# Optimization experiments

Measured on AMD Instinct MI355X. Metric: run time of the kernel, lower is better.

The kernel has to match this reference:

```python
import jax, jax.numpy as jnp
import numpy as np

K = 2
BN_EPS = 1e-5


def setup_inputs() -> dict:
    key = jax.random.key(0)
    k1, k2, k3 = jax.random.split(key, 3)
    B, C, H, W, D, O = 4, 128, 32, 32, 32, 128
    x = jax.random.normal(k1, (B, C, H, W, D), dtype=jnp.float32)
    conv_w = jax.random.normal(k2, (O, 2 * C), dtype=jnp.float32) * 0.02  # 1x1x1 conv kernel
    conv_b = jax.random.normal(k3, (O,), dtype=jnp.float32) * 0.02
    bn_gamma = jnp.ones((O,), dtype=jnp.float32)
    bn_beta = jnp.zeros((O,), dtype=jnp.float32)
    return {"x": x, "conv_w": conv_w, "conv_b": conv_b,
            "bn_gamma": bn_gamma, "bn_beta": bn_beta}


def _axis_running_max(x, x_j, axis, dim):
    # torch.cat([x[..., -i:], x[..., :-i]], axis) == jnp.roll(x, i, axis)
    shifts = jnp.arange(K, dim, K)

    def step(carry, s):
        diff = x - jnp.roll(x, s, axis=axis)
        return jnp.maximum(carry, diff), None

    x_j, _ = jax.lax.scan(step, x_j, shifts)
    return x_j


def reference(x, conv_w, conv_b, bn_gamma, bn_beta):
    B, C, H, W, D = x.shape
    x_j = jnp.zeros_like(x)
    x_j = _axis_running_max(x, x_j, 2, H)
    x_j = _axis_running_max(x, x_j, 3, W)
    x_j = _axis_running_max(x, x_j, 4, D)
    x_j = jax.lax.stop_gradient(x_j)  # original detaches every x_j update

    xc = jnp.concatenate([x, x_j], axis=1)  # [B, 2C, H, W, D]
    # 1x1x1 Conv3d == per-voxel channel GEMM
    y = jnp.einsum('bchwd,oc->bohwd', xc, conv_w) + conv_b[None, :, None, None, None]

    # BatchNorm3d, training mode (batch statistics over B,H,W,D)
    mean = y.mean(axis=(0, 2, 3, 4), keepdims=True)
    var = ((y - mean) ** 2).mean(axis=(0, 2, 3, 4), keepdims=True)
    yn = (y - mean) * jax.lax.rsqrt(var + BN_EPS)
    yn = yn * bn_gamma[None, :, None, None, None] + bn_beta[None, :, None, None, None]

    # torch nn.GELU default is exact erf form
    return jax.nn.gelu(yn, approximate=False)
```

## Files before the change

### kernel.cpp

```cpp
#include <hip/hip_runtime.h>
#include <hip/hip_bf16.h>

#define BB 4
#define CCH 128
#define C2 256
#define OO 128
#define NVOX 32768
#define NTOT (BB*NVOX)

typedef __attribute__((ext_vector_type(4))) float f32x4;
typedef __attribute__((ext_vector_type(8))) short s16x8;
typedef __attribute__((ext_vector_type(4))) unsigned int u32x4;
typedef unsigned int u32;
typedef unsigned short u16;

#define SWZ(r) ((((r)>>3) ^ (r)) & 7)

__device__ __forceinline__ float bf2f(short s){
  union { u32 i; float f; } cv; cv.i = ((u32)(u16)s) << 16; return cv.f;
}
__device__ __forceinline__ short f2bf(float f){
  union { __hip_bfloat16 h; short s; } cv; cv.h = __float2bfloat16(f); return cv.s;
}
__device__ __forceinline__ u32 pack2(float a, float b){
  return ((u32)(u16)f2bf(a)) | (((u32)(u16)f2bf(b)) << 16);
}
__device__ __forceinline__ float ulo(u32 r){
  union { u32 i; float f; } cv; cv.i = r << 16; return cv.f;
}
__device__ __forceinline__ float uhi(u32 r){
  union { u32 i; float f; } cv; cv.i = r & 0xffff0000u; return cv.f;
}

__global__ __launch_bounds__(256) void k_convw(const float* __restrict__ w, short* __restrict__ wb){
  int i = blockIdx.x*256 + threadIdx.x;
  wb[i] = f2bf(w[i]);
}


__device__ __forceinline__ int swz3(int h, int w, int bin){
  int s1 = ((w>>1) ^ h) & 3;
  int s2 = ((w>>3) ^ (h>>2)) & 3;
  return (h<<11) + ((w ^ s2)<<6) + ((bin & 15) | (((((bin>>4)) ^ s1) & 3) << 4));
}

__global__ __launch_bounds__(256) void k_xj(const float* __restrict__ x, short* __restrict__ xc){
  __shared__ __align__(16) u32 xs[16384];
  __shared__ __align__(16) u32 tw[2048];
  __shared__ __align__(16) u32 th[2048];
  int t = threadIdx.x;
  u32 bc = blockIdx.x;
  const float* __restrict__ src = x + (size_t)bc*NVOX;

  #pragma unroll
  for(int j=0;j<32;j++){
    int e0 = (t + 256*j)*4;
    f32x4 v = *(const f32x4*)(src + e0);
    int h = e0>>10, w = (e0>>5)&31, bin = (e0&31)*2;
    u32* dst = (u32*)((char*)xs + swz3(h,w,bin));
    dst[0] = pack2(v[0], v[1]);
    dst[1] = pack2(v[2], v[3]);
  }
  __syncthreads();

  {
    int task = t & 127, dg = task & 3, aa = task >> 2;
    float m1[2][8], m2[2][8];
    #pragma unroll
    for(int p=0;p<2;p++)
      #pragma unroll
      for(int k=0;k<8;k++){ m1[p][k]=1e30f; m2[p][k]=1e30f; }
    if(t < 128){
      int h = aa;
      #pragma unroll
      for(int w=0;w<32;w++){
        int p = w & 1;
        u32x4 g = *(const u32x4*)((const char*)xs + swz3(h,w,dg<<4));
        #pragma unroll
        for(int q=0;q<4;q++){
          float a = ulo(g[q]), b = uhi(g[q]);
          m2[p][2*q]   = fminf(m2[p][2*q],   fmaxf(m1[p][2*q],   a)); m1[p][2*q]   = fminf(m1[p][2*q],   a);
          m2[p][2*q+1] = fminf(m2[p][2*q+1], fmaxf(m1[p][2*q+1], b)); m1[p][2*q+1] = fminf(m1[p][2*q+1], b);
        }
      }
      #pragma unroll
      for(int p=0;p<2;p++){
        u32 o[8];
        #pragma unroll
        for(int k=0;k<8;k++) o[k] = pack2(m1[p][k], m2[p][k]);
        u32* d0 = &tw[h*64 + p*32 + dg*8];
        *(u32x4*)d0     = (u32x4){o[0],o[1],o[2],o[3]};
        *(u32x4*)(d0+4) = (u32x4){o[4],o[5],o[6],o[7]};
      }
    } else {
      int w = aa;
      #pragma unroll
      for(int h=0;h<32;h++){
        int p = h & 1;
        u32x4 g = *(const u32x4*)((const char*)xs + swz3(h,w,dg<<4));
        #pragma unroll
        for(int q=0;q<4;q++){
          float a = ulo(g[q]), b = uhi(g[q]);
          m2[p][2*q]   = fminf(m2[p][2*q],   fmaxf(m1[p][2*q],   a)); m1[p][2*q]   = fminf(m1[p][2*q],   a);
          m2[p][2*q+1] = fminf(m2[p][2*q+1], fmaxf(m1[p][2*q+1], b)); m1[p][2*q+1] = fminf(m1[p][2*q+1], b);
        }
      }
      #pragma unroll
      for(int p=0;p<2;p++){
        u32 o[8];
        #pragma unroll
        for(int k=0;k<8;k++) o[k] = pack2(m1[p][k], m2[p][k]);
        int row = p*1024 + w*32;
        *(u32x4*)&th[row + (((2*dg  ) ^ (w&7))*4)] = (u32x4){o[0],o[1],o[2],o[3]};
        *(u32x4*)&th[row + (((2*dg+1) ^ (w&7))*4)] = (u32x4){o[4],o[5],o[6],o[7]};
      }
    }
  }
  __syncthreads();

  short* __restrict__ px = xc + ((size_t)((bc>>7)*C2 + (bc&127)))*NVOX;
  short* __restrict__ pj = px + (size_t)CCH*NVOX;
  #pragma unroll
  for(int j=0;j<4;j++){
    int l = t + 256*j;
    int h = l>>5, w = l&31;
    u32x4 xr[4];
    #pragma unroll
    for(int g=0;g<4;g++)
      xr[g] = *(const u32x4*)((const char*)xs + swz3(h,w,g<<4));
    float xv[32];
    #pragma unroll
    for(int g=0;g<4;g++)
      #pragma unroll
      for(int q=0;q<4;q++){
        xv[g*8+2*q]   = ulo(xr[g][q]);
        xv[g*8+2*q+1] = uhi(xr[g][q]);
      }
    float m1d[2] = {1e30f,1e30f}, m2d[2] = {1e30f,1e30f};
    #pragma unroll
    for(int q=0;q<16;q++){
      m2d[0] = fminf(m2d[0], fmaxf(m1d[0], xv[2*q]));   m1d[0] = fminf(m1d[0], xv[2*q]);
      m2d[1] = fminf(m2d[1], fmaxf(m1d[1], xv[2*q+1])); m1d[1] = fminf(m1d[1], xv[2*q+1]);
    }
    const u32* twr = &tw[h*64 + (w&1)*32];
    int thbase = (h&1)*1024 + w*32, ws7 = w&7;
    u32 xjp[16];
    #pragma unroll
    for(int q=0;q<8;q++){
      u32x4 wv = *(const u32x4*)(twr + q*4);
      u32x4 hv = *(const u32x4*)(&th[thbase + ((q ^ ws7)*4)]);
      float o4[4];
      #pragma unroll
      for(int i=0;i<4;i++){
        int d = q*4 + i, p = d & 1;
        float xvv = xv[d];
        float meD = (xvv == m1d[p]) ? m2d[p] : m1d[p];
        float w1 = ulo(wv[i]);
        float meW = (xvv == w1) ? uhi(wv[i]) : w1;
        float h1 = ulo(hv[i]);
        float meH = (xvv == h1) ? uhi(hv[i]) : h1;
        float m = fminf(meD, fminf(meW, meH));
        o4[i] = fmaxf(0.0f, xvv - m);
      }
      xjp[q*2]   = pack2(o4[0], o4[1]);
      xjp[q*2+1] = pack2(o4[2], o4[3]);
    }
    #pragma unroll
    for(int g=0;g<4;g++){
      *(u32x4*)(px + (size_t)l*32 + g*8) = xr[g];
      *(u32x4*)(pj + (size_t)l*32 + g*8) = (u32x4){xjp[g*4],xjp[g*4+1],xjp[g*4+2],xjp[g*4+3]};
    }
  }
}

__global__ __launch_bounds__(256) void k_gemm(const short* __restrict__ xc, const short* __restrict__ wb,
                                              short* __restrict__ y){
  __shared__ __align__(16) char lds[32768];
  u32 blk = blockIdx.x;
  u32 vblk = blk & 255, b = blk >> 8;
  u32 vbase = vblk * 128;
  const short* __restrict__ xb = xc + (size_t)b*C2*NVOX + vbase;
  int t = threadIdx.x;
  int wave = t >> 6, lane = t & 63;
  int wr = wave >> 1, wc = wave & 1;
  int l15 = lane & 15, l4 = lane >> 4;
  f32x4 acc[4][4];
  #pragma unroll
  for(int mt=0;mt<4;mt++)
    #pragma unroll
    for(int nt=0;nt<4;nt++) acc[mt][nt] = (f32x4){0.f,0.f,0.f,0.f};

  int v0  = (t & 15) * 8;
  int cb2 = 2 * (t >> 4);

  #pragma unroll
  for(int kc=0;kc<2;kc++){
    s16x8 ra[4], rb[4];
    #pragma unroll
    for(int q=0;q<4;q++){
      const short* src = xb + (size_t)(kc*128 + cb2 + 32*q)*NVOX + v0;
      ra[q] = *(const s16x8*)(src);
      rb[q] = *(const s16x8*)(src + NVOX);
    }
    __syncthreads();
    #pragma unroll
    for(int q=0;q<4;q++){
      int c = cb2 + 32*q;
      #pragma unroll
      for(int e=0;e<8;e++){
        int v = v0 + e;
        u32 pr = ((u32)(u16)ra[q][e]) | (((u32)(u16)rb[q][e]) << 16);
        *(u32*)(lds + v*256 + ((((c>>3) ^ SWZ(v))<<4) | ((c&7)<<1))) = pr;
      }
    }
    __syncthreads();
    #pragma unroll
    for(int ks=0;ks<4;ks++){
      int kk = ks*32 + l4*8;
      s16x8 afrag[4], bfrag[4];
      #pragma unroll
      for(int nt=0;nt<4;nt++){
        int vloc = wc*64 + nt*16 + l15;
        bfrag[nt] = *(const s16x8*)(lds + vloc*256 + (((kk>>3) ^ SWZ(vloc))<<4));
      }
      #pragma unroll
      for(int mt=0;mt<4;mt++){
        int o = wr*64 + mt*16 + l15;
        afrag[mt] = *(const s16x8*)(wb + o*C2 + kc*128 + kk);
      }
      #pragma unroll
      for(int mt=0;mt<4;mt++)
        #pragma unroll
        for(int nt=0;nt<4;nt++)
          acc[mt][nt] = __builtin_amdgcn_mfma_f32_16x16x32_bf16(afrag[mt], bfrag[nt], acc[mt][nt], 0,0,0);
    }
  }

  __syncthreads();
  #pragma unroll
  for(int mt=0;mt<4;mt++){
    #pragma unroll
    for(int nt=0;nt<4;nt++){
      int vcol = wc*64 + nt*16 + l15;
      #pragma unroll
      for(int r=0;r<4;r++){
        int o = wr*64 + mt*16 + l4*4 + r;
        *(short*)(lds + o*256 + ((((vcol>>3) ^ SWZ(o))<<4) | ((vcol&7)<<1))) = f2bf(acc[mt][nt][r]);
      }
    }
  }
  __syncthreads();
  short* __restrict__ yb = y + (size_t)b*OO*NVOX + vbase;
  #pragma unroll
  for(int q=0;q<8;q++){
    int p = t + q*256;
    int o = p >> 4, vs = (p & 15) * 8;
    s16x8 val = *(const s16x8*)(lds + o*256 + ((((vs>>3) ^ SWZ(o))<<4)));
    *(s16x8*)(yb + (size_t)o*NVOX + vs) = val;
  }
}

__global__ __launch_bounds__(256) void k_statsp(const short* __restrict__ y, float* __restrict__ part){
  int blk = blockIdx.x;
  int o = blk >> 3, s = blk & 7;
  int t = threadIdx.x;
  float sm = 0.f, ss = 0.f;
  for(int b=0;b<BB;b++){
    const short* p = y + ((size_t)b*OO + o)*NVOX + s*4096;
    #pragma unroll
    for(int it=0;it<2;it++){
      s16x8 u = *(const s16x8*)(p + (t + 256*it)*8);
      #pragma unroll
      for(int e=0;e<8;e++){ float f = bf2f(u[e]); sm += f; ss += f*f; }
    }
  }
  __shared__ float rs[256], rss[256];
  rs[t] = sm; rss[t] = ss;
  __syncthreads();
  for(int k=128;k>0;k>>=1){
    if(t<k){ rs[t]+=rs[t+k]; rss[t]+=rss[t+k]; }
    __syncthreads();
  }
  if(t==0){ part[2*blk] = rs[0]; part[2*blk+1] = rss[0]; }
}

__global__ __launch_bounds__(128) void k_statsf(const float* __restrict__ part, float* __restrict__ stats){
  int o = threadIdx.x;
  float sm = 0.f, ss = 0.f;
  #pragma unroll
  for(int s=0;s<8;s++){ sm += part[2*(o*8+s)]; ss += part[2*(o*8+s)+1]; }
  float inv = 1.0f/(float)NTOT;
  float mean = sm*inv;
  float var = ss*inv - mean*mean;
  stats[2*o]   = mean;
  stats[2*o+1] = rsqrtf(var + 1e-5f);
}

__global__ __launch_bounds__(256) void k_bngelu(const short* __restrict__ y, const float* __restrict__ stats,
                                                const float* __restrict__ gamma, const float* __restrict__ beta,
                                                float* __restrict__ out){
  size_t base = ((size_t)blockIdx.x*256 + threadIdx.x)*8;
  int o = (int)((base >> 15) & 127);
  float mean = stats[2*o], rstd = stats[2*o+1];
  float g  = gamma[o]*rstd;
  float be = beta[o] - mean*g;
  s16x8 u = *(const s16x8*)(y + base);
  f32x4 r0, r1;
  #pragma unroll
  for(int e=0;e<8;e++){
    float yn = bf2f(u[e])*g + be;
    float ge = 0.5f*yn*(1.0f + erff(yn*0.70710678118654752f));
    if(e<4) r0[e] = ge; else r1[e-4] = ge;
  }
  *(f32x4*)(out + base)     = r0;
  *(f32x4*)(out + base + 4) = r1;
}

extern "C" void kernel_launch(void* const* d_in, const int* in_sizes, int n_in,
                              void* d_out, int out_size, void* d_ws, size_t ws_size,
                              hipStream_t stream) {
  (void)in_sizes; (void)n_in; (void)out_size; (void)ws_size;
  const float* x     = (const float*)d_in[0];
  const float* cw    = (const float*)d_in[1];
  const float* gamma = (const float*)d_in[3];
  const float* beta  = (const float*)d_in[4];
  float* out = (float*)d_out;

  char* ws = (char*)d_ws;
  short* wb    = (short*)ws;
  short* y     = (short*)(ws + 65536);
  float* stats = (float*)(ws + 65536 + (size_t)BB*OO*NVOX*2);
  float* part  = stats + 256;
  short* xcbuf = (short*)d_out;

  k_convw <<<dim3((OO*C2)/256),     dim3(256), 0, stream>>>(cw, wb);
  k_xj    <<<dim3(BB*CCH),         dim3(256), 0, stream>>>(x, xcbuf);
  k_gemm  <<<dim3(BB*(NVOX/128)),  dim3(256), 0, stream>>>(xcbuf, wb, y);
  k_statsp<<<dim3(OO*8),           dim3(256), 0, stream>>>(y, part);
  k_statsf<<<dim3(1),              dim3(128), 0, stream>>>(part, stats);
  k_bngelu<<<dim3((NTOT*OO)/2048), dim3(256), 0, stream>>>(y, stats, gamma, beta, out);
}
```

Before: 100.4 us.

## Fuse BN statistics into GEMM epilogue and widen x_j kernel to 512 threads

The GEMM epilogue now computes per-channel partial sums and sums of squares from the bf16 tile already staged in LDS. It writes one partial per block and channel, which removes the separate k_statsp pass that re-read all of y from global memory. The final reduction kernel now uses one block per channel to reduce 1024 partials. Separately, k_xj runs with 512 threads per block, so each thread handles half as many H/W running-min lanes, giving more parallelism per block at the cost of higher register and LDS pressure per CU. The partial buffer grows to 1024x128x2 floats.

```diff
diff --git a/kernel.cpp b/kernel.cpp
--- a/kernel.cpp
+++ b/kernel.cpp
@@ -7,10 +7,12 @@
 #define OO 128
 #define NVOX 32768
 #define NTOT (BB*NVOX)
+#define NGB 1024
 
 typedef __attribute__((ext_vector_type(4))) float f32x4;
 typedef __attribute__((ext_vector_type(8))) short s16x8;
 typedef __attribute__((ext_vector_type(4))) unsigned int u32x4;
+typedef __attribute__((ext_vector_type(2))) unsigned int u32x2;
 typedef unsigned int u32;
 typedef unsigned short u16;
 
@@ -44,7 +46,7 @@
   return (h<<11) + ((w ^ s2)<<6) + ((bin & 15) | (((((bin>>4)) ^ s1) & 3) << 4));
 }
 
-__global__ __launch_bounds__(256) void k_xj(const float* __restrict__ x, short* __restrict__ xc){
+__global__ __launch_bounds__(512, 4) void k_xj(const float* __restrict__ x, short* __restrict__ xc){
   __shared__ __align__(16) u32 xs[16384];
   __shared__ __align__(16) u32 tw[2048];
   __shared__ __align__(16) u32 th[2048];
@@ -53,8 +55,8 @@
   const float* __restrict__ src = x + (size_t)bc*NVOX;
 
   #pragma unroll
-  for(int j=0;j<32;j++){
-    int e0 = (t + 256*j)*4;
+  for(int j=0;j<16;j++){
+    int e0 = (t + 512*j)*4;
     f32x4 v = *(const f32x4*)(src + e0);
     int h = e0>>10, w = (e0>>5)&31, bin = (e0&31)*2;
     u32* dst = (u32*)((char*)xs + swz3(h,w,bin));
@@ -64,20 +66,20 @@
   __syncthreads();
 
   {
-    int task = t & 127, dg = task & 3, aa = task >> 2;
-    float m1[2][8], m2[2][8];
+    int dq = t & 7, aa = (t >> 3) & 31;
+    float m1[2][4], m2[2][4];
     #pragma unroll
     for(int p=0;p<2;p++)
       #pragma unroll
-      for(int k=0;k<8;k++){ m1[p][k]=1e30f; m2[p][k]=1e30f; }
-    if(t < 128){
+      for(int k=0;k<4;k++){ m1[p][k]=1e30f; m2[p][k]=1e30f; }
+    if(t < 256){
       int h = aa;
       #pragma unroll
       for(int w=0;w<32;w++){
         int p = w & 1;
-        u32x4 g = *(const u32x4*)((const char*)xs + swz3(h,w,dg<<4));
+        u32x2 g = *(const u32x2*)((const char*)xs + swz3(h,w,dq*8));
         #pragma unroll
-        for(int q=0;q<4;q++){
+        for(int q=0;q<2;q++){
           float a = ulo(g[q]), b = uhi(g[q]);
           m2[p][2*q]   = fminf(m2[p][2*q],   fmaxf(m1[p][2*q],   a)); m1[p][2*q]   = fminf(m1[p][2*q],   a);
           m2[p][2*q+1] = fminf(m2[p][2*q+1], fmaxf(m1[p][2*q+1], b)); m1[p][2*q+1] = fminf(m1[p][2*q+1], b);
@@ -85,21 +87,18 @@
       }
       #pragma unroll
       for(int p=0;p<2;p++){
-        u32 o[8];
-        #pragma unroll
-        for(int k=0;k<8;k++) o[k] = pack2(m1[p][k], m2[p][k]);
-        u32* d0 = &tw[h*64 + p*32 + dg*8];
-        *(u32x4*)d0     = (u32x4){o[0],o[1],o[2],o[3]};
-        *(u32x4*)(d0+4) = (u32x4){o[4],o[5],o[6],o[7]};
+        u32 o0 = pack2(m1[p][0], m2[p][0]), o1 = pack2(m1[p][1], m2[p][1]);
+        u32 o2 = pack2(m1[p][2], m2[p][2]), o3 = pack2(m1[p][3], m2[p][3]);
+        *(u32x4*)&tw[h*64 + p*32 + dq*4] = (u32x4){o0,o1,o2,o3};
       }
     } else {
       int w = aa;
       #pragma unroll
       for(int h=0;h<32;h++){
         int p = h & 1;
-        u32x4 g = *(const u32x4*)((const char*)xs + swz3(h,w,dg<<4));
+        u32x2 g = *(const u32x2*)((const char*)xs + swz3(h,w,dq*8));
         #pragma unroll
-        for(int q=0;q<4;q++){
+        for(int q=0;q<2;q++){
           float a = ulo(g[q]), b = uhi(g[q]);
           m2[p][2*q]   = fminf(m2[p][2*q],   fmaxf(m1[p][2*q],   a)); m1[p][2*q]   = fminf(m1[p][2*q],   a);
           m2[p][2*q+1] = fminf(m2[p][2*q+1], fmaxf(m1[p][2*q+1], b)); m1[p][2*q+1] = fminf(m1[p][2*q+1], b);
@@ -107,12 +106,9 @@
       }
       #pragma unroll
       for(int p=0;p<2;p++){
-        u32 o[8];
-        #pragma unroll
-        for(int k=0;k<8;k++) o[k] = pack2(m1[p][k], m2[p][k]);
-        int row = p*1024 + w*32;
-        *(u32x4*)&th[row + (((2*dg  ) ^ (w&7))*4)] = (u32x4){o[0],o[1],o[2],o[3]};
-        *(u32x4*)&th[row + (((2*dg+1) ^ (w&7))*4)] = (u32x4){o[4],o[5],o[6],o[7]};
+        u32 o0 = pack2(m1[p][0], m2[p][0]), o1 = pack2(m1[p][1], m2[p][1]);
+        u32 o2 = pack2(m1[p][2], m2[p][2]), o3 = pack2(m1[p][3], m2[p][3]);
+        *(u32x4*)&th[p*1024 + w*32 + ((dq ^ (w&7))*4)] = (u32x4){o0,o1,o2,o3};
       }
     }
   }
@@ -121,8 +117,8 @@
   short* __restrict__ px = xc + ((size_t)((bc>>7)*C2 + (bc&127)))*NVOX;
   short* __restrict__ pj = px + (size_t)CCH*NVOX;
   #pragma unroll
-  for(int j=0;j<4;j++){
-    int l = t + 256*j;
+  for(int j=0;j<2;j++){
+    int l = t + 512*j;
     int h = l>>5, w = l&31;
     u32x4 xr[4];
     #pragma unroll
@@ -174,7 +170,7 @@
 }
 
 __global__ __launch_bounds__(256) void k_gemm(const short* __restrict__ xc, const short* __restrict__ wb,
-                                              short* __restrict__ y){
+                                              short* __restrict__ y, float* __restrict__ part){
   __shared__ __align__(16) char lds[32768];
   u32 blk = blockIdx.x;
   u32 vblk = blk & 255, b = blk >> 8;
@@ -258,21 +254,34 @@
     s16x8 val = *(const s16x8*)(lds + o*256 + ((((vs>>3) ^ SWZ(o))<<4)));
     *(s16x8*)(yb + (size_t)o*NVOX + vs) = val;
   }
-}
-
-__global__ __launch_bounds__(256) void k_statsp(const short* __restrict__ y, float* __restrict__ part){
-  int blk = blockIdx.x;
-  int o = blk >> 3, s = blk & 7;
-  int t = threadIdx.x;
+
+  {
+    int o = t >> 1, vh = t & 1;
+    float sm = 0.f, ss = 0.f;
+    #pragma unroll
+    for(int k=0;k<8;k++){
+      int vs = vh*64 + k*8;
+      s16x8 val = *(const s16x8*)(lds + o*256 + ((((vs>>3) ^ SWZ(o))<<4)));
+      #pragma unroll
+      for(int e=0;e<8;e++){ float f = bf2f(val[e]); sm += f; ss += f*f; }
+    }
+    sm += __shfl_xor(sm, 1);
+    ss += __shfl_xor(ss, 1);
+    if(vh == 0){
+      float* pp = part + ((size_t)blk*OO + o)*2;
+      pp[0] = sm; pp[1] = ss;
+    }
+  }
+}
+
+__global__ __launch_bounds__(256) void k_statsf(const float* __restrict__ part, float* __restrict__ stats){
+  int o = blockIdx.x, t = threadIdx.x;
   float sm = 0.f, ss = 0.f;
-  for(int b=0;b<BB;b++){
-    const short* p = y + ((size_t)b*OO + o)*NVOX + s*4096;
-    #pragma unroll
-    for(int it=0;it<2;it++){
-      s16x8 u = *(const s16x8*)(p + (t + 256*it)*8);
-      #pragma unroll
-      for(int e=0;e<8;e++){ float f = bf2f(u[e]); sm += f; ss += f*f; }
-    }
+  #pragma unroll
+  for(int k=0;k<4;k++){
+    int blk = t + k*256;
+    const float* pp = part + ((size_t)blk*OO + o)*2;
+    sm += pp[0]; ss += pp[1];
   }
   __shared__ float rs[256], rss[256];
   rs[t] = sm; rss[t] = ss;
@@ -281,19 +290,13 @@
     if(t<k){ rs[t]+=rs[t+k]; rss[t]+=rss[t+k]; }
     __syncthreads();
   }
-  if(t==0){ part[2*blk] = rs[0]; part[2*blk+1] = rss[0]; }
-}
-
-__global__ __launch_bounds__(128) void k_statsf(const float* __restrict__ part, float* __restrict__ stats){
-  int o = threadIdx.x;
-  float sm = 0.f, ss = 0.f;
-  #pragma unroll
-  for(int s=0;s<8;s++){ sm += part[2*(o*8+s)]; ss += part[2*(o*8+s)+1]; }
-  float inv = 1.0f/(float)NTOT;
-  float mean = sm*inv;
-  float var = ss*inv - mean*mean;
-  stats[2*o]   = mean;
-  stats[2*o+1] = rsqrtf(var + 1e-5f);
+  if(t==0){
+    float inv = 1.0f/(float)NTOT;
+    float mean = rs[0]*inv;
+    float var = rss[0]*inv - mean*mean;
+    stats[2*o]   = mean;
+    stats[2*o+1] = rsqrtf(var + 1e-5f);
+  }
 }
 
 __global__ __launch_bounds__(256) void k_bngelu(const short* __restrict__ y, const float* __restrict__ stats,
@@ -334,9 +337,8 @@
   short* xcbuf = (short*)d_out;
 
   k_convw <<<dim3((OO*C2)/256),     dim3(256), 0, stream>>>(cw, wb);
-  k_xj    <<<dim3(BB*CCH),         dim3(256), 0, stream>>>(x, xcbuf);
-  k_gemm  <<<dim3(BB*(NVOX/128)),  dim3(256), 0, stream>>>(xcbuf, wb, y);
-  k_statsp<<<dim3(OO*8),           dim3(256), 0, stream>>>(y, part);
-  k_statsf<<<dim3(1),              dim3(128), 0, stream>>>(part, stats);
+  k_xj    <<<dim3(BB*CCH),         dim3(512), 0, stream>>>(x, xcbuf);
+  k_gemm  <<<dim3(BB*(NVOX/128)),  dim3(256), 0, stream>>>(xcbuf, wb, y, part);
+  k_statsf<<<dim3(OO),             dim3(256), 0, stream>>>(part, stats);
   k_bngelu<<<dim3((NTOT*OO)/2048), dim3(256), 0, stream>>>(y, stats, gamma, beta, out);
 }
```

Result: no change. 98.80 us (-1.6%).
